# Performance work log

Hardware: AMD Instinct MI355X
Metric: run time of the kernel (lower is better)

The kernel has to match this reference:

```python
import jax, jax.numpy as jnp
import numpy as np

DIM = 1024
HID = 4096
E = 8
K = 3


def setup_inputs() -> dict:
    key = jax.random.key(0)
    ks = jax.random.split(key, 5)
    x = jax.random.normal(ks[0], (2, 2048, DIM), dtype=jnp.float32)
    # router: nn.Linear(dim, E) -- initialized to zero in source, but we use small
    # random weights so routing is non-degenerate for the correctness baseline.
    router_w = jax.random.normal(ks[1], (E, DIM), dtype=jnp.float32) * 0.02
    router_b = jax.random.normal(ks[2], (E,), dtype=jnp.float32) * 0.02
    # per-expert SwiGLU params: w12: [E, dim, 2*hid], w3: [E, hid, dim]
    w12 = jax.random.normal(ks[3], (E, DIM, 2 * HID), dtype=jnp.float32) * 0.02
    w3 = jax.random.normal(ks[4], (E, HID, DIM), dtype=jnp.float32) * 0.02
    return {"x": x, "router_w": router_w, "router_b": router_b, "w12": w12, "w3": w3}


def _moe(x, router_w, router_b, w12, w3):
    # router logits [B, S, E]
    logits = jnp.einsum("bsd,ed->bse", x, router_w) + router_b
    scores = jax.nn.sigmoid(logits)
    topk_scores, topk_idx = jax.lax.top_k(scores, K)  # [B,S,K]
    weights = topk_scores / (topk_scores.sum(axis=-1, keepdims=True) + 1e-6)
    # dense per-expert combine weight [B, S, E] (zero if expert not selected)
    onehot = jax.nn.one_hot(topk_idx, E, dtype=x.dtype)  # [B,S,K,E]
    dense_w = jnp.einsum("bske,bsk->bse", onehot, weights)
    out = jnp.zeros_like(x)
    for e in range(E):  # small fixed structural loop over experts
        x12 = x @ w12[e]  # [B,S,2H]
        x1, x2 = jnp.split(x12, 2, axis=-1)
        hidden = jax.nn.silu(x1) * x2
        out = out + (hidden @ w3[e]) * dense_w[..., e:e + 1]
    aux_loss = 0.01 * jnp.mean(logits ** 2)
    return out, aux_loss


def reference(x, router_w, router_b, w12, w3):
    return _moe(x, router_w, router_b, w12, w3)
```

## Files before the change

### kernel.cpp

```cpp
#include <hip/hip_runtime.h>
#include <math.h>

typedef unsigned short u16;
typedef __bf16 bf16x8 __attribute__((ext_vector_type(8)));
typedef float f32x4 __attribute__((ext_vector_type(4)));

#define T_TOK 4096
#define DIM   1024
#define HID   4096
#define NE    8
#define TOPK  3
#define NPAIR 12288

constexpr size_t OFF_CTRL = 0;
constexpr size_t OFF_XB   = 256;
constexpr size_t OFF_W12T = OFF_XB   + (size_t)T_TOK * DIM * 2;
constexpr size_t OFF_W3T  = OFF_W12T + (size_t)NE * 2 * HID * DIM * 2;
constexpr size_t OFF_HID  = OFF_W3T  + (size_t)NE * DIM * HID * 2;
constexpr size_t OFF_Y    = OFF_HID  + (size_t)NPAIR * HID * 2;
constexpr size_t OFF_PTOK = OFF_Y    + (size_t)NPAIR * DIM * 4;
constexpr size_t OFF_TE   = OFF_PTOK + (size_t)NPAIR * 4;
constexpr size_t OFF_TW   = OFF_TE   + (size_t)T_TOK * TOPK * 4;
constexpr size_t OFF_TS   = OFF_TW   + (size_t)T_TOK * TOPK * 4;

__device__ __forceinline__ u16 f2bf(float f) {
    unsigned u = __builtin_bit_cast(unsigned, f);
    u += 0x7fffu + ((u >> 16) & 1u);
    return (u16)(u >> 16);
}

__device__ __forceinline__ void ld_g2l(const u16* g, u16* l) {
    __builtin_amdgcn_global_load_lds((__attribute__((address_space(1))) unsigned*)(g),
                                     (__attribute__((address_space(3))) unsigned*)(l),
                                     16, 0, 0);
}

#define VMCNT0 asm volatile("s_waitcnt vmcnt(0)" ::: "memory")
#define LGKM0  asm volatile("s_waitcnt lgkmcnt(0)" ::: "memory")
#define SBAR   __builtin_amdgcn_s_barrier()
#define SCHED0 __builtin_amdgcn_sched_barrier(0)

#define STAGE8(dst)                                                    \
  {                                                                    \
    _Pragma("unroll")                                                  \
    for (int r_ = 0; r_ < 4; ++r_)                                     \
      ld_g2l(srcA[r_], (dst) + (r_ * 64 + wave * 8) * 64);             \
    _Pragma("unroll")                                                  \
    for (int r_ = 0; r_ < 4; ++r_)                                     \
      ld_g2l(srcB[r_], (dst) + 16384 + (r_ * 64 + wave * 8) * 64);     \
    _Pragma("unroll")                                                  \
    for (int r_ = 0; r_ < 4; ++r_) { srcA[r_] += 64; srcB[r_] += 64; } \
  }

__global__ __launch_bounds__(256) void transpose_cast_kernel(const float* __restrict__ in,
                                                             u16* __restrict__ out, int K, int N) {
    __shared__ float tile[64][33];
    const float* inp = in + (size_t)blockIdx.z * K * N;
    u16* outp = out + (size_t)blockIdx.z * K * N;
    const int n0 = blockIdx.x * 32, k0 = blockIdx.y * 64;
    const int tid = threadIdx.x;
#pragma unroll
    for (int i = 0; i < 2; ++i) {
        int k = i * 32 + (tid >> 3);
        int c4 = (tid & 7) * 4;
        float4 f = *(const float4*)(inp + (size_t)(k0 + k) * N + n0 + c4);
        tile[k][c4 + 0] = f.x; tile[k][c4 + 1] = f.y;
        tile[k][c4 + 2] = f.z; tile[k][c4 + 3] = f.w;
    }
    __syncthreads();
    const int n = tid >> 3, c = (tid & 7) * 8;
    u16 buf[8];
#pragma unroll
    for (int j = 0; j < 8; ++j) buf[j] = f2bf(tile[c + j][n]);
    *(uint4*)(outp + (size_t)(n0 + n) * K + k0 + c) = *(uint4*)buf;
}

__global__ __launch_bounds__(256) void router_kernel(const float* __restrict__ x,
                                                     const float* __restrict__ rw,
                                                     const float* __restrict__ rb,
                                                     u16* __restrict__ xb,
                                                     int* __restrict__ tok_expert,
                                                     float* __restrict__ tok_w,
                                                     int* __restrict__ ctrl,
                                                     float* __restrict__ aux) {
    __shared__ int hist[NE];
    __shared__ float auxsh;
    const int tid = threadIdx.x;
    if (tid < NE) hist[tid] = 0;
    if (tid == NE) auxsh = 0.f;
    __syncthreads();

    const int wave = tid >> 6, lane = tid & 63;
    const int t = blockIdx.x * 4 + wave;
    const float* xr = x + (size_t)t * DIM;
    u16* xbr = xb + (size_t)t * DIM;

    float p[NE];
#pragma unroll
    for (int e = 0; e < NE; e++) p[e] = 0.f;
#pragma unroll
    for (int q = 0; q < 4; ++q) {
        const int d = q * 256 + lane * 4;
        float4 f = *(const float4*)(xr + d);
        uint2 v;
        v.x = (unsigned)f2bf(f.x) | ((unsigned)f2bf(f.y) << 16);
        v.y = (unsigned)f2bf(f.z) | ((unsigned)f2bf(f.w) << 16);
        *(uint2*)(xbr + d) = v;
#pragma unroll
        for (int e = 0; e < NE; e++) {
            float4 w = *(const float4*)(rw + e * DIM + d);
            p[e] += f.x * w.x + f.y * w.y + f.z * w.z + f.w * w.w;
        }
    }
#pragma unroll
    for (int e = 0; e < NE; e++) {
#pragma unroll
        for (int off = 32; off; off >>= 1) p[e] += __shfl_down(p[e], off, 64);
    }
    if (lane == 0) {
        float s[NE]; float auxs = 0.f;
#pragma unroll
        for (int e = 0; e < NE; e++) {
            float lg = p[e] + rb[e];
            auxs += lg * lg;
            s[e] = 1.f / (1.f + __expf(-lg));
        }
        atomicAdd(&auxsh, auxs);
        unsigned mask = 0; float wsum = 0.f;
        int idxs[TOPK]; float vals[TOPK];
        for (int k = 0; k < TOPK; k++) {
            float best = -1.f; int bi = 0;
            for (int e = 0; e < NE; e++)
                if (!((mask >> e) & 1u) && s[e] > best) { best = s[e]; bi = e; }
            mask |= 1u << bi; idxs[k] = bi; vals[k] = best; wsum += best;
        }
        wsum += 1e-6f;
        for (int k = 0; k < TOPK; k++) {
            tok_expert[t * TOPK + k] = idxs[k];
            tok_w[t * TOPK + k] = vals[k] / wsum;
            atomicAdd(&hist[idxs[k]], 1);
        }
    }
    __syncthreads();
    if (tid < NE) { int h = hist[tid]; if (h) atomicAdd(&ctrl[tid], h); }
    if (tid == NE) atomicAdd(aux, auxsh * (0.01f / 32768.0f));
}

__global__ void scan_kernel(int* __restrict__ ctrl) {
    if (threadIdx.x == 0) {
        int acc = 0;
        for (int e = 0; e < NE; e++) { ctrl[8 + e] = acc; acc += ctrl[e]; }
    }
}

__global__ __launch_bounds__(256) void assign_kernel(const int* __restrict__ tok_expert,
                                                     const float* __restrict__ tok_w,
                                                     int* __restrict__ ctrl,
                                                     int* __restrict__ pair_token,
                                                     int* __restrict__ tok_slot) {
    int t = blockIdx.x * blockDim.x + threadIdx.x;
    if (t >= T_TOK) return;
    for (int k = 0; k < TOPK; k++) {
        int e = tok_expert[t * TOPK + k];
        int pos = atomicAdd(&ctrl[16 + e], 1);
        int slot = ctrl[8 + e] + pos;
        pair_token[slot] = t;
        tok_slot[t * TOPK + k] = slot;
    }
}

__global__ __launch_bounds__(512, 2) void gemm1_kernel(const u16* __restrict__ xb,
                                                       const u16* __restrict__ w12t,
                                                       const int* __restrict__ pair_token,
                                                       const int* __restrict__ ctrl,
                                                       u16* __restrict__ hidden) {
    const int e = blockIdx.z;
    const int cnt = ctrl[e];
    if ((int)blockIdx.y * 256 >= cnt) return;
    const int off = ctrl[8 + e];
    const int rowbase = off + blockIdx.y * 256;
    const int rowend = off + cnt;
    const int n0 = blockIdx.x * 128;

    extern __shared__ __align__(16) u16 lds[];

    const int tid = threadIdx.x;
    const int wave = tid >> 6, lane = tid & 63;
    const int srow = tid >> 3;
    const int scol = ((tid & 7) ^ (srow & 7)) * 8;

    const u16* srcA[4];
    const u16* srcB[4];
#pragma unroll
    for (int r = 0; r < 4; ++r) {
        int sr = rowbase + r * 64 + srow;
        int tok = (sr < rowend) ? pair_token[sr] : 0;
        srcA[r] = xb + (size_t)tok * DIM + scol;
    }
#pragma unroll
    for (int r = 0; r < 2; ++r) {
        srcB[r]     = w12t + ((size_t)e * 2 * HID + n0 + r * 64 + srow) * DIM + scol;
        srcB[r + 2] = srcB[r] + (size_t)HID * DIM;
    }

    const int wm = wave >> 2, wn = wave & 3;
    const int lrow = lane & 15, lq = lane >> 4, xm = lrow & 7;
    const int so0 = ((lq ^ xm) << 3);
    const int so1 = (((4 | lq) ^ xm) << 3);

    f32x4 acc0[8][2], acc1[8][2];
#pragma unroll
    for (int mf = 0; mf < 8; ++mf)
#pragma unroll
        for (int nf = 0; nf < 2; ++nf) { acc0[mf][nf] = (f32x4)0.f; acc1[mf][nf] = (f32x4)0.f; }

    STAGE8(lds);
    VMCNT0; SBAR;

    for (int kt = 0; kt < 16; ++kt) {
        u16* sl = lds + (kt & 1) * 32768;
        u16* sn = lds + ((kt & 1) ^ 1) * 32768;
        const u16* sA = sl;
        const u16* sB = sl + 16384;
        if (kt < 15) STAGE8(sn);

        bf16x8 a[4][2], b0[2][2], b1[2][2];
#pragma unroll
        for (int mf = 0; mf < 4; ++mf) {
            const u16* base = sA + (wm * 128 + mf * 16 + lrow) * 64;
            a[mf][0] = *(const bf16x8*)(base + so0);
            a[mf][1] = *(const bf16x8*)(base + so1);
        }
#pragma unroll
        for (int nf = 0; nf < 2; ++nf) {
            const u16* base = sB + (wn * 32 + nf * 16 + lrow) * 64;
            b0[nf][0] = *(const bf16x8*)(base + so0);
            b0[nf][1] = *(const bf16x8*)(base + so1);
        }
        SBAR; LGKM0; SCHED0;
        __builtin_amdgcn_s_setprio(1);
#pragma unroll
        for (int mf = 0; mf < 4; ++mf)
#pragma unroll
            for (int nf = 0; nf < 2; ++nf) {
                acc0[mf][nf] = __builtin_amdgcn_mfma_f32_16x16x32_bf16(a[mf][0], b0[nf][0], acc0[mf][nf], 0, 0, 0);
                acc0[mf][nf] = __builtin_amdgcn_mfma_f32_16x16x32_bf16(a[mf][1], b0[nf][1], acc0[mf][nf], 0, 0, 0);
            }
        __builtin_amdgcn_s_setprio(0);
        SBAR;
#pragma unroll
        for (int nf = 0; nf < 2; ++nf) {
            const u16* base = sB + 128 * 64 + (wn * 32 + nf * 16 + lrow) * 64;
            b1[nf][0] = *(const bf16x8*)(base + so0);
            b1[nf][1] = *(const bf16x8*)(base + so1);
        }
        SBAR; LGKM0; SCHED0;
        __builtin_amdgcn_s_setprio(1);
#pragma unroll
        for (int mf = 0; mf < 4; ++mf)
#pragma unroll
            for (int nf = 0; nf < 2; ++nf) {
                acc1[mf][nf] = __builtin_amdgcn_mfma_f32_16x16x32_bf16(a[mf][0], b1[nf][0], acc1[mf][nf], 0, 0, 0);
                acc1[mf][nf] = __builtin_amdgcn_mfma_f32_16x16x32_bf16(a[mf][1], b1[nf][1], acc1[mf][nf], 0, 0, 0);
            }
        __builtin_amdgcn_s_setprio(0);
        SBAR;
#pragma unroll
        for (int mf = 0; mf < 4; ++mf) {
            const u16* base = sA + (wm * 128 + (mf + 4) * 16 + lrow) * 64;
            a[mf][0] = *(const bf16x8*)(base + so0);
            a[mf][1] = *(const bf16x8*)(base + so1);
        }
        SBAR; LGKM0; SCHED0;
        __builtin_amdgcn_s_setprio(1);
#pragma unroll
        for (int mf = 0; mf < 4; ++mf)
#pragma unroll
            for (int nf = 0; nf < 2; ++nf) {
                acc1[mf + 4][nf] = __builtin_amdgcn_mfma_f32_16x16x32_bf16(a[mf][0], b1[nf][0], acc1[mf + 4][nf], 0, 0, 0);
                acc1[mf + 4][nf] = __builtin_amdgcn_mfma_f32_16x16x32_bf16(a[mf][1], b1[nf][1], acc1[mf + 4][nf], 0, 0, 0);
            }
        __builtin_amdgcn_s_setprio(0);
        SBAR;
        __builtin_amdgcn_s_setprio(1);
#pragma unroll
        for (int mf = 0; mf < 4; ++mf)
#pragma unroll
            for (int nf = 0; nf < 2; ++nf) {
                acc0[mf + 4][nf] = __builtin_amdgcn_mfma_f32_16x16x32_bf16(a[mf][0], b0[nf][0], acc0[mf + 4][nf], 0, 0, 0);
                acc0[mf + 4][nf] = __builtin_amdgcn_mfma_f32_16x16x32_bf16(a[mf][1], b0[nf][1], acc0[mf + 4][nf], 0, 0, 0);
            }
        __builtin_amdgcn_s_setprio(0);
        VMCNT0; SBAR;
    }

#pragma unroll
    for (int mf = 0; mf < 8; ++mf) {
        const int gr0 = rowbase + wm * 128 + mf * 16 + lq * 4;
#pragma unroll
        for (int nf = 0; nf < 2; ++nf) {
            const int gc = n0 + wn * 32 + nf * 16 + lrow;
#pragma unroll
            for (int r = 0; r < 4; ++r) {
                const int gr = gr0 + r;
                if (gr < rowend) {
                    float x1 = acc0[mf][nf][r], x2 = acc1[mf][nf][r];
                    float h = x1 / (1.f + __expf(-x1)) * x2;
                    hidden[(size_t)gr * HID + gc] = f2bf(h);
                }
            }
        }
    }
}

__global__ __launch_bounds__(512, 2) void gemm2_kernel(const u16* __restrict__ hidden,
                                                       const u16* __restrict__ w3t,
                                                       const int* __restrict__ ctrl,
                                                       float* __restrict__ ybuf) {
    const int e = blockIdx.z;
    const int cnt = ctrl[e];
    if ((int)blockIdx.y * 256 >= cnt) return;
    const int off = ctrl[8 + e];
    const int rowbase = off + blockIdx.y * 256;
    const int rowend = off + cnt;
    const int n0 = blockIdx.x * 256;

    extern __shared__ __align__(16) u16 lds[];

    const int tid = threadIdx.x;
    const int wave = tid >> 6, lane = tid & 63;
    const int srow = tid >> 3;
    const int scol = ((tid & 7) ^ (srow & 7)) * 8;

    const u16* srcA[4];
    const u16* srcB[4];
#pragma unroll
    for (int r = 0; r < 4; ++r) {
        int sr = rowbase + r * 64 + srow;
        if (sr > NPAIR - 1) sr = NPAIR - 1;
        srcA[r] = hidden + (size_t)sr * HID + scol;
        srcB[r] = w3t + ((size_t)e * DIM + n0 + r * 64 + srow) * HID + scol;
    }

    const int wm = wave >> 2, wn = wave & 3;
    const int lrow = lane & 15, lq = lane >> 4, xm = lrow & 7;
    const int so0 = ((lq ^ xm) << 3);
    const int so1 = (((4 | lq) ^ xm) << 3);

    f32x4 acc[8][4];
#pragma unroll
    for (int mf = 0; mf < 8; ++mf)
#pragma unroll
        for (int nf = 0; nf < 4; ++nf) acc[mf][nf] = (f32x4)0.f;

    STAGE8(lds);
    VMCNT0; SBAR;

    for (int kt = 0; kt < 64; ++kt) {
        u16* sl = lds + (kt & 1) * 32768;
        u16* sn = lds + ((kt & 1) ^ 1) * 32768;
        const u16* sA = sl;
        const u16* sB = sl + 16384;
        if (kt < 63) STAGE8(sn);

        bf16x8 a[4][2], b[4][2];
#pragma unroll
        for (int mf = 0; mf < 4; ++mf) {
            const u16* base = sA + (wm * 128 + mf * 16 + lrow) * 64;
            a[mf][0] = *(const bf16x8*)(base + so0);
            a[mf][1] = *(const bf16x8*)(base + so1);
        }
#pragma unroll
        for (int nf = 0; nf < 2; ++nf) {
            const u16* base = sB + (wn * 64 + nf * 16 + lrow) * 64;
            b[nf][0] = *(const bf16x8*)(base + so0);
            b[nf][1] = *(const bf16x8*)(base + so1);
        }
        SBAR; LGKM0; SCHED0;
        __builtin_amdgcn_s_setprio(1);
#pragma unroll
        for (int mf = 0; mf < 4; ++mf)
#pragma unroll
            for (int nf = 0; nf < 2; ++nf) {
                acc[mf][nf] = __builtin_amdgcn_mfma_f32_16x16x32_bf16(a[mf][0], b[nf][0], acc[mf][nf], 0, 0, 0);
                acc[mf][nf] = __builtin_amdgcn_mfma_f32_16x16x32_bf16(a[mf][1], b[nf][1], acc[mf][nf], 0, 0, 0);
            }
        __builtin_amdgcn_s_setprio(0);
        SBAR;
#pragma unroll
        for (int nf = 2; nf < 4; ++nf) {
            const u16* base = sB + (wn * 64 + nf * 16 + lrow) * 64;
            b[nf][0] = *(const bf16x8*)(base + so0);
            b[nf][1] = *(const bf16x8*)(base + so1);
        }
        SBAR; LGKM0; SCHED0;
        __builtin_amdgcn_s_setprio(1);
#pragma unroll
        for (int mf = 0; mf < 4; ++mf)
#pragma unroll
            for (int nf = 2; nf < 4; ++nf) {
                acc[mf][nf] = __builtin_amdgcn_mfma_f32_16x16x32_bf16(a[mf][0], b[nf][0], acc[mf][nf], 0, 0, 0);
                acc[mf][nf] = __builtin_amdgcn_mfma_f32_16x16x32_bf16(a[mf][1], b[nf][1], acc[mf][nf], 0, 0, 0);
            }
        __builtin_amdgcn_s_setprio(0);
        SBAR;
#pragma unroll
        for (int mf = 0; mf < 4; ++mf) {
            const u16* base = sA + (wm * 128 + (mf + 4) * 16 + lrow) * 64;
            a[mf][0] = *(const bf16x8*)(base + so0);
            a[mf][1] = *(const bf16x8*)(base + so1);
        }
        SBAR; LGKM0; SCHED0;
        __builtin_amdgcn_s_setprio(1);
#pragma unroll
        for (int mf = 0; mf < 4; ++mf)
#pragma unroll
            for (int nf = 2; nf < 4; ++nf) {
                acc[mf + 4][nf] = __builtin_amdgcn_mfma_f32_16x16x32_bf16(a[mf][0], b[nf][0], acc[mf + 4][nf], 0, 0, 0);
                acc[mf + 4][nf] = __builtin_amdgcn_mfma_f32_16x16x32_bf16(a[mf][1], b[nf][1], acc[mf + 4][nf], 0, 0, 0);
            }
        __builtin_amdgcn_s_setprio(0);
        SBAR;
        __builtin_amdgcn_s_setprio(1);
#pragma unroll
        for (int mf = 0; mf < 4; ++mf)
#pragma unroll
            for (int nf = 0; nf < 2; ++nf) {
                acc[mf + 4][nf] = __builtin_amdgcn_mfma_f32_16x16x32_bf16(a[mf][0], b[nf][0], acc[mf + 4][nf], 0, 0, 0);
                acc[mf + 4][nf] = __builtin_amdgcn_mfma_f32_16x16x32_bf16(a[mf][1], b[nf][1], acc[mf + 4][nf], 0, 0, 0);
            }
        __builtin_amdgcn_s_setprio(0);
        VMCNT0; SBAR;
    }

#pragma unroll
    for (int mf = 0; mf < 8; ++mf) {
        const int gr0 = rowbase + wm * 128 + mf * 16 + lq * 4;
#pragma unroll
        for (int nf = 0; nf < 4; ++nf) {
            const int gc = n0 + wn * 64 + nf * 16 + lrow;
#pragma unroll
            for (int r = 0; r < 4; ++r) {
                const int gr = gr0 + r;
                if (gr < rowend) ybuf[(size_t)gr * DIM + gc] = acc[mf][nf][r];
            }
        }
    }
}

__global__ __launch_bounds__(256) void combine_kernel(const float* __restrict__ ybuf,
                                                      const int* __restrict__ tok_slot,
                                                      const float* __restrict__ tok_w,
                                                      float* __restrict__ out) {
    const int t = blockIdx.x;
    const int d = threadIdx.x * 4;
    const int s0 = tok_slot[t * 3 + 0], s1 = tok_slot[t * 3 + 1], s2 = tok_slot[t * 3 + 2];
    const float w0 = tok_w[t * 3 + 0], w1 = tok_w[t * 3 + 1], w2 = tok_w[t * 3 + 2];
    const float4 a0 = *(const float4*)(ybuf + (size_t)s0 * DIM + d);
    const float4 a1 = *(const float4*)(ybuf + (size_t)s1 * DIM + d);
    const float4 a2 = *(const float4*)(ybuf + (size_t)s2 * DIM + d);
    float4 o;
    o.x = w0 * a0.x + w1 * a1.x + w2 * a2.x;
    o.y = w0 * a0.y + w1 * a1.y + w2 * a2.y;
    o.z = w0 * a0.z + w1 * a1.z + w2 * a2.z;
    o.w = w0 * a0.w + w1 * a1.w + w2 * a2.w;
    *(float4*)(out + (size_t)t * DIM + d) = o;
}

extern "C" void kernel_launch(void* const* d_in, const int* in_sizes, int n_in,
                              void* d_out, int out_size, void* d_ws, size_t ws_size,
                              hipStream_t stream) {
    const float* x   = (const float*)d_in[0];
    const float* rw  = (const float*)d_in[1];
    const float* rb  = (const float*)d_in[2];
    const float* w12 = (const float*)d_in[3];
    const float* w3  = (const float*)d_in[4];
    float* out = (float*)d_out;
    char* ws = (char*)d_ws;

    int*   ctrl       = (int*)(ws + OFF_CTRL);
    u16*   xb         = (u16*)(ws + OFF_XB);
    u16*   w12t       = (u16*)(ws + OFF_W12T);
    u16*   w3t        = (u16*)(ws + OFF_W3T);
    u16*   hidden     = (u16*)(ws + OFF_HID);
    float* ybuf       = (float*)(ws + OFF_Y);
    int*   pair_token = (int*)(ws + OFF_PTOK);
    int*   tok_expert = (int*)(ws + OFF_TE);
    float* tok_w      = (float*)(ws + OFF_TW);
    int*   tok_slot   = (int*)(ws + OFF_TS);

    static bool attr_set = false;
    if (!attr_set) {
        hipFuncSetAttribute((const void*)gemm1_kernel, hipFuncAttributeMaxDynamicSharedMemorySize, 131072);
        hipFuncSetAttribute((const void*)gemm2_kernel, hipFuncAttributeMaxDynamicSharedMemorySize, 131072);
        attr_set = true;
    }

    hipMemsetAsync(ctrl, 0, 256, stream);
    hipMemsetAsync(out + (size_t)T_TOK * DIM, 0, sizeof(float), stream);

    router_kernel<<<T_TOK / 4, 256, 0, stream>>>(x, rw, rb, xb, tok_expert, tok_w, ctrl,
                                                 out + (size_t)T_TOK * DIM);
    transpose_cast_kernel<<<dim3(2 * HID / 32, DIM / 64, NE), 256, 0, stream>>>(w12, w12t, DIM, 2 * HID);
    transpose_cast_kernel<<<dim3(DIM / 32, HID / 64, NE), 256, 0, stream>>>(w3, w3t, HID, DIM);
    scan_kernel<<<1, 64, 0, stream>>>(ctrl);
    assign_kernel<<<16, 256, 0, stream>>>(tok_expert, tok_w, ctrl, pair_token, tok_slot);

    gemm1_kernel<<<dim3(HID / 128, 16, NE), 512, 131072, stream>>>(xb, w12t, pair_token, ctrl, hidden);
    gemm2_kernel<<<dim3(DIM / 256, 16, NE), 512, 131072, stream>>>(hidden, w3t, ctrl, ybuf);
    combine_kernel<<<T_TOK, 256, 0, stream>>>(ybuf, tok_slot, tok_w, out);
    (void)in_sizes; (void)n_in; (void)out_size; (void)ws_size;
}
```

Before: 964.8 us.

## Split next-tile global-to-LDS loads into chunks interleaved with MFMA phases

Both grouped GEMM kernels now issue the next K-tile's global-to-LDS loads in three chunks, each placed right after the LDS region it overwrites has been read, rather than all at once at the top of the iteration. Partial vmcnt waits replace the full vmcnt(0) at the end of each iteration, and two redundant barriers are removed. This is meant to keep more memory traffic in flight during MFMA work and cut stall time at barriers. The down-projection kernel also changes each wave's B-column mapping to an interleaved layout, which could alter LDS bank behaviour and store coalescing. The hand-tuned vmcnt counts are fragile and must match the exact load ordering.

```diff
diff --git a/kernel.cpp b/kernel.cpp
--- a/kernel.cpp
+++ b/kernel.cpp
@@ -35,22 +35,23 @@
                                      16, 0, 0);
 }
 
-#define VMCNT0 asm volatile("s_waitcnt vmcnt(0)" ::: "memory")
+#define VMCNT(N) asm volatile("s_waitcnt vmcnt(" #N ")" ::: "memory")
 #define LGKM0  asm volatile("s_waitcnt lgkmcnt(0)" ::: "memory")
 #define SBAR   __builtin_amdgcn_s_barrier()
 #define SCHED0 __builtin_amdgcn_sched_barrier(0)
-
-#define STAGE8(dst)                                                    \
-  {                                                                    \
-    _Pragma("unroll")                                                  \
-    for (int r_ = 0; r_ < 4; ++r_)                                     \
-      ld_g2l(srcA[r_], (dst) + (r_ * 64 + wave * 8) * 64);             \
-    _Pragma("unroll")                                                  \
-    for (int r_ = 0; r_ < 4; ++r_)                                     \
-      ld_g2l(srcB[r_], (dst) + 16384 + (r_ * 64 + wave * 8) * 64);     \
-    _Pragma("unroll")                                                  \
-    for (int r_ = 0; r_ < 4; ++r_) { srcA[r_] += 64; srcB[r_] += 64; } \
-  }
+#define PRIO1  __builtin_amdgcn_s_setprio(1)
+#define PRIO0  __builtin_amdgcn_s_setprio(0)
+
+#define STAGE_A02(dst) { ld_g2l(srcA[0], (dst) + (0 * 64 + wave * 8) * 64); \
+                         ld_g2l(srcA[2], (dst) + (2 * 64 + wave * 8) * 64); }
+#define STAGE_B01(dst) { ld_g2l(srcB[0], (dst) + 16384 + (0 * 64 + wave * 8) * 64); \
+                         ld_g2l(srcB[1], (dst) + 16384 + (1 * 64 + wave * 8) * 64); }
+#define STAGE_B23(dst) { ld_g2l(srcB[2], (dst) + 16384 + (2 * 64 + wave * 8) * 64); \
+                         ld_g2l(srcB[3], (dst) + 16384 + (3 * 64 + wave * 8) * 64); }
+#define STAGE_A13(dst) { ld_g2l(srcA[1], (dst) + (1 * 64 + wave * 8) * 64); \
+                         ld_g2l(srcA[3], (dst) + (3 * 64 + wave * 8) * 64); }
+#define ADV()          { _Pragma("unroll") \
+                         for (int r_ = 0; r_ < 4; ++r_) { srcA[r_] += 64; srcB[r_] += 64; } }
 
 __global__ __launch_bounds__(256) void transpose_cast_kernel(const float* __restrict__ in,
                                                              u16* __restrict__ out, int K, int N) {
@@ -214,17 +215,21 @@
 #pragma unroll
         for (int nf = 0; nf < 2; ++nf) { acc0[mf][nf] = (f32x4)0.f; acc1[mf][nf] = (f32x4)0.f; }
 
-    STAGE8(lds);
-    VMCNT0; SBAR;
-
-    for (int kt = 0; kt < 16; ++kt) {
-        u16* sl = lds + (kt & 1) * 32768;
-        u16* sn = lds + ((kt & 1) ^ 1) * 32768;
-        const u16* sA = sl;
-        const u16* sB = sl + 16384;
-        if (kt < 15) STAGE8(sn);
+    STAGE_A02(lds); STAGE_B01(lds);
+    STAGE_B23(lds);
+    STAGE_A13(lds);
+    ADV();
+
+    const int NT = DIM / 64;
+    for (int kt = 0; kt < NT; ++kt) {
+        u16* cur = lds + (kt & 1) * 32768;
+        u16* nxt = lds + ((kt & 1) ^ 1) * 32768;
+        const u16* sA = cur;
+        const u16* sB = cur + 16384;
+        const bool notlast = (kt < NT - 1);
 
         bf16x8 a[4][2], b0[2][2], b1[2][2];
+        VMCNT(4); SBAR; SCHED0;
 #pragma unroll
         for (int mf = 0; mf < 4; ++mf) {
             const u16* base = sA + (wm * 128 + mf * 16 + lrow) * 64;
@@ -237,8 +242,9 @@
             b0[nf][0] = *(const bf16x8*)(base + so0);
             b0[nf][1] = *(const bf16x8*)(base + so1);
         }
-        SBAR; LGKM0; SCHED0;
-        __builtin_amdgcn_s_setprio(1);
+        if (notlast) { STAGE_A02(nxt); STAGE_B01(nxt); }
+        LGKM0; SCHED0;
+        PRIO1;
 #pragma unroll
         for (int mf = 0; mf < 4; ++mf)
 #pragma unroll
@@ -246,16 +252,18 @@
                 acc0[mf][nf] = __builtin_amdgcn_mfma_f32_16x16x32_bf16(a[mf][0], b0[nf][0], acc0[mf][nf], 0, 0, 0);
                 acc0[mf][nf] = __builtin_amdgcn_mfma_f32_16x16x32_bf16(a[mf][1], b0[nf][1], acc0[mf][nf], 0, 0, 0);
             }
-        __builtin_amdgcn_s_setprio(0);
-        SBAR;
+        PRIO0;
+        if (notlast) { VMCNT(6); } else { VMCNT(2); }
+        SBAR; SCHED0;
 #pragma unroll
         for (int nf = 0; nf < 2; ++nf) {
             const u16* base = sB + 128 * 64 + (wn * 32 + nf * 16 + lrow) * 64;
             b1[nf][0] = *(const bf16x8*)(base + so0);
             b1[nf][1] = *(const bf16x8*)(base + so1);
         }
-        SBAR; LGKM0; SCHED0;
-        __builtin_amdgcn_s_setprio(1);
+        if (notlast) STAGE_B23(nxt);
+        LGKM0; SCHED0;
+        PRIO1;
 #pragma unroll
         for (int mf = 0; mf < 4; ++mf)
 #pragma unroll
@@ -263,16 +271,18 @@
                 acc1[mf][nf] = __builtin_amdgcn_mfma_f32_16x16x32_bf16(a[mf][0], b1[nf][0], acc1[mf][nf], 0, 0, 0);
                 acc1[mf][nf] = __builtin_amdgcn_mfma_f32_16x16x32_bf16(a[mf][1], b1[nf][1], acc1[mf][nf], 0, 0, 0);
             }
-        __builtin_amdgcn_s_setprio(0);
-        SBAR;
+        PRIO0;
+        if (notlast) { VMCNT(6); } else { VMCNT(0); }
+        SBAR; SCHED0;
 #pragma unroll
         for (int mf = 0; mf < 4; ++mf) {
             const u16* base = sA + (wm * 128 + (mf + 4) * 16 + lrow) * 64;
             a[mf][0] = *(const bf16x8*)(base + so0);
             a[mf][1] = *(const bf16x8*)(base + so1);
         }
-        SBAR; LGKM0; SCHED0;
-        __builtin_amdgcn_s_setprio(1);
+        if (notlast) { STAGE_A13(nxt); ADV(); }
+        LGKM0; SCHED0;
+        PRIO1;
 #pragma unroll
         for (int mf = 0; mf < 4; ++mf)
 #pragma unroll
@@ -280,9 +290,9 @@
                 acc1[mf + 4][nf] = __builtin_amdgcn_mfma_f32_16x16x32_bf16(a[mf][0], b1[nf][0], acc1[mf + 4][nf], 0, 0, 0);
                 acc1[mf + 4][nf] = __builtin_amdgcn_mfma_f32_16x16x32_bf16(a[mf][1], b1[nf][1], acc1[mf + 4][nf], 0, 0, 0);
             }
-        __builtin_amdgcn_s_setprio(0);
+        PRIO0;
         SBAR;
-        __builtin_amdgcn_s_setprio(1);
+        PRIO1;
 #pragma unroll
         for (int mf = 0; mf < 4; ++mf)
 #pragma unroll
@@ -290,8 +300,7 @@
                 acc0[mf + 4][nf] = __builtin_amdgcn_mfma_f32_16x16x32_bf16(a[mf][0], b0[nf][0], acc0[mf + 4][nf], 0, 0, 0);
                 acc0[mf + 4][nf] = __builtin_amdgcn_mfma_f32_16x16x32_bf16(a[mf][1], b0[nf][1], acc0[mf + 4][nf], 0, 0, 0);
             }
-        __builtin_amdgcn_s_setprio(0);
-        VMCNT0; SBAR;
+        PRIO0;
     }
 
 #pragma unroll
@@ -353,17 +362,21 @@
 #pragma unroll
         for (int nf = 0; nf < 4; ++nf) acc[mf][nf] = (f32x4)0.f;
 
-    STAGE8(lds);
-    VMCNT0; SBAR;
-
-    for (int kt = 0; kt < 64; ++kt) {
-        u16* sl = lds + (kt & 1) * 32768;
-        u16* sn = lds + ((kt & 1) ^ 1) * 32768;
-        const u16* sA = sl;
-        const u16* sB = sl + 16384;
-        if (kt < 63) STAGE8(sn);
+    STAGE_A02(lds); STAGE_B01(lds);
+    STAGE_B23(lds);
+    STAGE_A13(lds);
+    ADV();
+
+    const int NT = HID / 64;
+    for (int kt = 0; kt < NT; ++kt) {
+        u16* cur = lds + (kt & 1) * 32768;
+        u16* nxt = lds + ((kt & 1) ^ 1) * 32768;
+        const u16* sA = cur;
+        const u16* sB = cur + 16384;
+        const bool notlast = (kt < NT - 1);
 
         bf16x8 a[4][2], b[4][2];
+        VMCNT(4); SBAR; SCHED0;
 #pragma unroll
         for (int mf = 0; mf < 4; ++mf) {
             const u16* base = sA + (wm * 128 + mf * 16 + lrow) * 64;
@@ -372,12 +385,13 @@
         }
 #pragma unroll
         for (int nf = 0; nf < 2; ++nf) {
-            const u16* base = sB + (wn * 64 + nf * 16 + lrow) * 64;
+            const u16* base = sB + (nf * 64 + wn * 16 + lrow) * 64;
             b[nf][0] = *(const bf16x8*)(base + so0);
             b[nf][1] = *(const bf16x8*)(base + so1);
         }
-        SBAR; LGKM0; SCHED0;
-        __builtin_amdgcn_s_setprio(1);
+        if (notlast) { STAGE_A02(nxt); STAGE_B01(nxt); }
+        LGKM0; SCHED0;
+        PRIO1;
 #pragma unroll
         for (int mf = 0; mf < 4; ++mf)
 #pragma unroll
@@ -385,16 +399,18 @@
                 acc[mf][nf] = __builtin_amdgcn_mfma_f32_16x16x32_bf16(a[mf][0], b[nf][0], acc[mf][nf], 0, 0, 0);
                 acc[mf][nf] = __builtin_amdgcn_mfma_f32_16x16x32_bf16(a[mf][1], b[nf][1], acc[mf][nf], 0, 0, 0);
             }
-        __builtin_amdgcn_s_setprio(0);
-        SBAR;
+        PRIO0;
+        if (notlast) { VMCNT(6); } else { VMCNT(2); }
+        SBAR; SCHED0;
 #pragma unroll
         for (int nf = 2; nf < 4; ++nf) {
-            const u16* base = sB + (wn * 64 + nf * 16 + lrow) * 64;
+            const u16* base = sB + (nf * 64 + wn * 16 + lrow) * 64;
             b[nf][0] = *(const bf16x8*)(base + so0);
             b[nf][1] = *(const bf16x8*)(base + so1);
         }
-        SBAR; LGKM0; SCHED0;
-        __builtin_amdgcn_s_setprio(1);
+        if (notlast) STAGE_B23(nxt);
+        LGKM0; SCHED0;
+        PRIO1;
 #pragma unroll
         for (int mf = 0; mf < 4; ++mf)
 #pragma unroll
@@ -402,16 +418,18 @@
                 acc[mf][nf] = __builtin_amdgcn_mfma_f32_16x16x32_bf16(a[mf][0], b[nf][0], acc[mf][nf], 0, 0, 0);
                 acc[mf][nf] = __builtin_amdgcn_mfma_f32_16x16x32_bf16(a[mf][1], b[nf][1], acc[mf][nf], 0, 0, 0);
             }
-        __builtin_amdgcn_s_setprio(0);
-        SBAR;
+        PRIO0;
+        if (notlast) { VMCNT(6); } else { VMCNT(0); }
+        SBAR; SCHED0;
 #pragma unroll
         for (int mf = 0; mf < 4; ++mf) {
             const u16* base = sA + (wm * 128 + (mf + 4) * 16 + lrow) * 64;
             a[mf][0] = *(const bf16x8*)(base + so0);
             a[mf][1] = *(const bf16x8*)(base + so1);
         }
-        SBAR; LGKM0; SCHED0;
-        __builtin_amdgcn_s_setprio(1);
+        if (notlast) { STAGE_A13(nxt); ADV(); }
+        LGKM0; SCHED0;
+        PRIO1;
 #pragma unroll
         for (int mf = 0; mf < 4; ++mf)
 #pragma unroll
@@ -419,9 +437,9 @@
                 acc[mf + 4][nf] = __builtin_amdgcn_mfma_f32_16x16x32_bf16(a[mf][0], b[nf][0], acc[mf + 4][nf], 0, 0, 0);
                 acc[mf + 4][nf] = __builtin_amdgcn_mfma_f32_16x16x32_bf16(a[mf][1], b[nf][1], acc[mf + 4][nf], 0, 0, 0);
             }
-        __builtin_amdgcn_s_setprio(0);
+        PRIO0;
         SBAR;
-        __builtin_amdgcn_s_setprio(1);
+        PRIO1;
 #pragma unroll
         for (int mf = 0; mf < 4; ++mf)
 #pragma unroll
@@ -429,8 +447,7 @@
                 acc[mf + 4][nf] = __builtin_amdgcn_mfma_f32_16x16x32_bf16(a[mf][0], b[nf][0], acc[mf + 4][nf], 0, 0, 0);
                 acc[mf + 4][nf] = __builtin_amdgcn_mfma_f32_16x16x32_bf16(a[mf][1], b[nf][1], acc[mf + 4][nf], 0, 0, 0);
             }
-        __builtin_amdgcn_s_setprio(0);
-        VMCNT0; SBAR;
+        PRIO0;
     }
 
 #pragma unroll
@@ -438,7 +455,7 @@
         const int gr0 = rowbase + wm * 128 + mf * 16 + lq * 4;
 #pragma unroll
         for (int nf = 0; nf < 4; ++nf) {
-            const int gc = n0 + wn * 64 + nf * 16 + lrow;
+            const int gc = n0 + nf * 64 + wn * 16 + lrow;
 #pragma unroll
             for (int r = 0; r < 4; ++r) {
                 const int gr = gr0 + r;
```

New measurement: 894.5 us. 1.08x faster.
